# Kernel tuning notes

Measured on AMD Instinct MI355X. Metric: run time of the kernel, lower is better.

Reference implementation:

```python
import jax, jax.numpy as jnp
import numpy as np

K = 3  # kernel size, stride=1, padding=0 (hardcoded in SingleAdder)


def setup_inputs() -> dict:
    key = jax.random.key(0)
    x = jax.random.normal(key, (16, 5, 512, 512), dtype=jnp.float32)
    # adder weight is initialized to all-ones in SingleAdder.__init__
    W = jnp.ones((5, 5, 3, 3), dtype=jnp.float32)
    return {"x": x, "W": W}


def adder2d(x, W):
    """AdderNet conv: out[n,co,i,j] = -sum_{ci,kh,kw} |x[n,ci,i+kh,j+kw] - W[co,ci,kh,kw]|.
    Loop over the 9 fixed kernel taps (not data dims); each tap is fully vectorized.
    Avoids materializing a full im2col tensor."""
    B, Ci, H, Wd = x.shape
    Co = W.shape[0]
    Ho, Wo = H - K + 1, Wd - K + 1
    out = jnp.zeros((B, Co, Ho, Wo), dtype=x.dtype)
    for kh in range(K):
        for kw in range(K):
            patch = x[:, None, :, kh:kh + Ho, kw:kw + Wo]        # [B,1,Ci,Ho,Wo]
            w = W[None, :, :, kh, kw, None, None]                # [1,Co,Ci,1,1]
            out = out - jnp.sum(jnp.abs(patch - w), axis=2)      # reduce over Ci
    return out


def reference(x, W):
    return adder2d(x, W)
```

## Files before the change

kernel.cpp:

```cpp
#include <hip/hip_runtime.h>


#define KK 3
#define NB 16
#define CI 5
#define CO 5
#define H 512
#define WD 512
#define HO 510
#define WO 510
#define TW 64
#define TH 16

__global__ __launch_bounds__(256)
void adder2d_kernel(const float* __restrict__ x,
                    const float* __restrict__ Wg,
                    float* __restrict__ out) {
    const int tx = threadIdx.x & 63;
    const int ty = threadIdx.x >> 6;
    const int j0 = blockIdx.x * TW;
    const int i0 = blockIdx.y * TH;
    const int n  = blockIdx.z;

    const int j     = j0 + tx;
    const int ibase = i0 + ty * 4;

    const int jc = j < WO ? j : (WO - 1);
    int rowoff[6];
    #pragma unroll
    for (int r = 0; r < 6; ++r) {
        int gi = ibase + r;
        gi = gi < H ? gi : (H - 1);
        rowoff[r] = gi * WD;
    }

    const float* xn = x + (size_t)n * CI * H * WD + jc;

    float acc[CO][4];
    #pragma unroll
    for (int co = 0; co < CO; ++co)
        #pragma unroll
        for (int r = 0; r < 4; ++r) acc[co][r] = 0.f;

    #pragma unroll 1
    for (int ci = 0; ci < CI; ++ci) {
        const float* p = xn + (size_t)ci * H * WD;
        float xw[6][KK];
        #pragma unroll
        for (int r = 0; r < 6; ++r) {
            const float* rp = p + rowoff[r];
            xw[r][0] = rp[0];
            xw[r][1] = rp[1];
            xw[r][2] = rp[2];
        }
        const float* wp = Wg + ci * (KK * KK);
        #pragma unroll
        for (int kh = 0; kh < KK; ++kh) {
            #pragma unroll
            for (int kw = 0; kw < KK; ++kw) {
                const int widx = kh * KK + kw;
                float w0 = wp[0 * 45 + widx];
                float w1 = wp[1 * 45 + widx];
                float w2 = wp[2 * 45 + widx];
                float w3 = wp[3 * 45 + widx];
                float w4 = wp[4 * 45 + widx];
                #pragma unroll
                for (int r = 0; r < 4; ++r) {
                    const float xv = xw[kh + r][kw];
                    acc[0][r] += fabsf(xv - w0);
                    acc[1][r] += fabsf(xv - w1);
                    acc[2][r] += fabsf(xv - w2);
                    acc[3][r] += fabsf(xv - w3);
                    acc[4][r] += fabsf(xv - w4);
                }
            }
        }
    }

    if (j < WO) {
        float* outn = out + (size_t)n * CO * HO * WO;
        #pragma unroll
        for (int co = 0; co < CO; ++co) {
            float* outc = outn + (size_t)co * HO * WO;
            #pragma unroll
            for (int r = 0; r < 4; ++r) {
                const int i = ibase + r;
                if (i < HO) outc[(size_t)i * WO + j] = -acc[co][r];
            }
        }
    }
}

extern "C" void kernel_launch(void* const* d_in, const int* in_sizes, int n_in,
                              void* d_out, int out_size, void* d_ws, size_t ws_size,
                              hipStream_t stream) {
    const float* x  = (const float*)d_in[0];
    const float* Wg = (const float*)d_in[1];
    float* out      = (float*)d_out;

    dim3 grid((WO + TW - 1) / TW,
              (HO + TH - 1) / TH,
              NB);
    dim3 block(256);
    adder2d_kernel<<<grid, block, 0, stream>>>(x, Wg, out);
}
```

Measured before the change: 166.7 us.

## Vectorize loads and stores with 4x2 per-thread output tiles

Each thread now computes four adjacent columns by two rows instead of one column by four rows. Inputs are read with float4/float2 vector loads and outputs written as float2 stores, and the block tile becomes 256x8. This cuts scalar load instruction count and the redundant overlap between columns. The halo overhead across rows goes up (4 input rows for 2 outputs), so more input bytes are loaded per output. Occupancy is also pinned with a launch-bounds hint.

```diff
diff --git a/kernel.cpp b/kernel.cpp
--- a/kernel.cpp
+++ b/kernel.cpp
@@ -9,10 +9,10 @@
 #define WD 512
 #define HO 510
 #define WO 510
-#define TW 64
-#define TH 16
+#define TW 256
+#define TH 8
 
-__global__ __launch_bounds__(256)
+__global__ __launch_bounds__(256, 4)
 void adder2d_kernel(const float* __restrict__ x,
                     const float* __restrict__ Wg,
                     float* __restrict__ out) {
@@ -22,36 +22,39 @@
     const int i0 = blockIdx.y * TH;
     const int n  = blockIdx.z;
 
-    const int j     = j0 + tx;
-    const int ibase = i0 + ty * 4;
+    const int j     = j0 + tx * 4;
+    const int ibase = i0 + ty * 2;
 
-    const int jc = j < WO ? j : (WO - 1);
-    int rowoff[6];
+    int rowoff[4];
     #pragma unroll
-    for (int r = 0; r < 6; ++r) {
+    for (int r = 0; r < 4; ++r) {
         int gi = ibase + r;
         gi = gi < H ? gi : (H - 1);
         rowoff[r] = gi * WD;
     }
+    const int j2 = (j + 4 <= WD - 2) ? (j + 4) : (WD - 2);
 
-    const float* xn = x + (size_t)n * CI * H * WD + jc;
+    const float* xn = x + (size_t)n * CI * H * WD;
 
-    float acc[CO][4];
+    float acc[CO][2][4];
     #pragma unroll
     for (int co = 0; co < CO; ++co)
         #pragma unroll
-        for (int r = 0; r < 4; ++r) acc[co][r] = 0.f;
+        for (int r = 0; r < 2; ++r)
+            #pragma unroll
+            for (int c = 0; c < 4; ++c) acc[co][r][c] = 0.f;
 
     #pragma unroll 1
     for (int ci = 0; ci < CI; ++ci) {
         const float* p = xn + (size_t)ci * H * WD;
-        float xw[6][KK];
+        float win[4][6];
         #pragma unroll
-        for (int r = 0; r < 6; ++r) {
+        for (int r = 0; r < 4; ++r) {
             const float* rp = p + rowoff[r];
-            xw[r][0] = rp[0];
-            xw[r][1] = rp[1];
-            xw[r][2] = rp[2];
+            const float4 a = *(const float4*)(rp + j);
+            const float2 b = *(const float2*)(rp + j2);
+            win[r][0] = a.x; win[r][1] = a.y; win[r][2] = a.z; win[r][3] = a.w;
+            win[r][4] = b.x; win[r][5] = b.y;
         }
         const float* wp = Wg + ci * (KK * KK);
         #pragma unroll
@@ -59,33 +62,40 @@
             #pragma unroll
             for (int kw = 0; kw < KK; ++kw) {
                 const int widx = kh * KK + kw;
-                float w0 = wp[0 * 45 + widx];
-                float w1 = wp[1 * 45 + widx];
-                float w2 = wp[2 * 45 + widx];
-                float w3 = wp[3 * 45 + widx];
-                float w4 = wp[4 * 45 + widx];
+                const float w0 = wp[0 * 45 + widx];
+                const float w1 = wp[1 * 45 + widx];
+                const float w2 = wp[2 * 45 + widx];
+                const float w3 = wp[3 * 45 + widx];
+                const float w4 = wp[4 * 45 + widx];
                 #pragma unroll
-                for (int r = 0; r < 4; ++r) {
-                    const float xv = xw[kh + r][kw];
-                    acc[0][r] += fabsf(xv - w0);
-                    acc[1][r] += fabsf(xv - w1);
-                    acc[2][r] += fabsf(xv - w2);
-                    acc[3][r] += fabsf(xv - w3);
-                    acc[4][r] += fabsf(xv - w4);
+                for (int r = 0; r < 2; ++r) {
+                    #pragma unroll
+                    for (int c = 0; c < 4; ++c) {
+                        const float xv = win[kh + r][kw + c];
+                        acc[0][r][c] += fabsf(xv - w0);
+                        acc[1][r][c] += fabsf(xv - w1);
+                        acc[2][r][c] += fabsf(xv - w2);
+                        acc[3][r][c] += fabsf(xv - w3);
+                        acc[4][r][c] += fabsf(xv - w4);
+                    }
                 }
             }
         }
     }
 
-    if (j < WO) {
-        float* outn = out + (size_t)n * CO * HO * WO;
+    const bool hi_ok = (j + 3) < WO;
+    float* outn = out + (size_t)n * CO * HO * WO;
+    #pragma unroll
+    for (int co = 0; co < CO; ++co) {
+        float* outc = outn + (size_t)co * HO * WO;
         #pragma unroll
-        for (int co = 0; co < CO; ++co) {
-            float* outc = outn + (size_t)co * HO * WO;
-            #pragma unroll
-            for (int r = 0; r < 4; ++r) {
-                const int i = ibase + r;
-                if (i < HO) outc[(size_t)i * WO + j] = -acc[co][r];
+        for (int r = 0; r < 2; ++r) {
+            const int i = ibase + r;
+            if (i < HO) {
+                float* op = outc + (size_t)i * WO + j;
+                *(float2*)(op)     = make_float2(-acc[co][r][0], -acc[co][r][1]);
+                if (hi_ok)
+                    *(float2*)(op + 2) = make_float2(-acc[co][r][2], -acc[co][r][3]);
             }
         }
     }
```

After: 191.9 us. 1.15x slower.
